# Kernel optimization log

Hardware: AMD Instinct MI355X
Metric: run time of the kernel (lower is better)

Reference implementation:

```python
import jax, jax.numpy as jnp
import numpy as np

B, T, R = 64, 256, 256          # batch, timepoints, n_rois (T==R required by bmm path)
H, NH, DH, FF, LAT, L = 256, 8, 32, 512, 64, 2
EPS = 1e-5


def layernorm(x, g, b):
    m = x.mean(-1, keepdims=True)
    v = ((x - m) ** 2).mean(-1, keepdims=True)
    return (x - m) / jnp.sqrt(v + EPS) * g + b


def leaky_relu(x):
    return jnp.where(x >= 0, x, 0.1 * x)


def setup_inputs() -> dict:
    key = jax.random.key(0)
    ks = iter(jax.random.split(key, 64))
    def nrm(shape, s=0.02):
        return jax.random.normal(next(ks), shape, jnp.float32) * s
    return {
        "x": jax.random.normal(next(ks), (B, T, R), jnp.float32),
        "node_view": jax.random.normal(next(ks), (B, R, R), jnp.float32) * 0.1,
        "edge_view": jax.random.normal(next(ks), (B, R, R), jnp.float32) * 0.1,
        "fp_w": nrm((H, R)), "fp_b": jnp.zeros((H,)),
        "fp_g": jnp.ones((H,)), "fp_beta": jnp.zeros((H,)),
        "qkv_w": nrm((L, 3 * H, H)), "qkv_b": jnp.zeros((L, 3 * H)),
        "attn_out_w": nrm((L, H, H)), "attn_out_b": jnp.zeros((L, H)),
        "ln1_g": jnp.ones((L, H)), "ln1_b": jnp.zeros((L, H)),
        "ff1_w": nrm((L, FF, H)), "ff1_b": jnp.zeros((L, FF)),
        "ff2_w": nrm((L, H, FF)), "ff2_b": jnp.zeros((L, H)),
        "ln2_g": jnp.ones((L, H)), "ln2_b": jnp.zeros((L, H)),
        "out_w": nrm((R, H)), "out_b": jnp.zeros((R,)),
        "mu_w1": nrm((H // 2, H)), "mu_b1": jnp.zeros((H // 2,)),
        "mu_g": jnp.ones((H // 2,)), "mu_beta": jnp.zeros((H // 2,)),
        "mu_w2": nrm((LAT, H // 2)), "mu_b2": jnp.zeros((LAT,)),
        "lv_w1": nrm((H // 2, H)), "lv_b1": jnp.zeros((H // 2,)),
        "lv_g": jnp.ones((H // 2,)), "lv_beta": jnp.zeros((H // 2,)),
        "lv_w2": nrm((LAT, H // 2)), "lv_b2": jnp.zeros((LAT,)),
    }


def reference(x, node_view, edge_view, fp_w, fp_b, fp_g, fp_beta,
              qkv_w, qkv_b, attn_out_w, attn_out_b, ln1_g, ln1_b,
              ff1_w, ff1_b, ff2_w, ff2_b, ln2_g, ln2_b,
              out_w, out_b, mu_w1, mu_b1, mu_g, mu_beta, mu_w2, mu_b2,
              lv_w1, lv_b1, lv_g, lv_beta, lv_w2, lv_b2):
    # graph-view message passing: bmm(x^T, view), averaged, transposed back
    xr = jnp.swapaxes(x, 1, 2)                           # [B,R,T]
    msg = 0.5 * (jnp.einsum('brt,btq->brq', xr, node_view)
                 + jnp.einsum('brt,btq->brq', xr, edge_view))
    h = jnp.swapaxes(msg, 1, 2)                          # [B,T,R]
    # feature_proj: Linear -> LayerNorm -> LeakyReLU(0.1) -> Dropout(eval)
    h = leaky_relu(layernorm(h @ fp_w.T + fp_b, fp_g, fp_beta))  # [B,T,H]
    # TransformerEncoder (post-norm, relu FFN, dropout=identity)
    scale = 1.0 / jnp.sqrt(jnp.float32(DH))
    for i in range(L):
        qkv = h @ qkv_w[i].T + qkv_b[i]                  # [B,T,3H]
        q, k, v = jnp.split(qkv, 3, axis=-1)
        q = q.reshape(B, T, NH, DH).transpose(0, 2, 1, 3)
        k = k.reshape(B, T, NH, DH).transpose(0, 2, 1, 3)
        v = v.reshape(B, T, NH, DH).transpose(0, 2, 1, 3)
        attn = jax.nn.softmax(jnp.einsum('bhqd,bhkd->bhqk', q, k) * scale, axis=-1)
        o = jnp.einsum('bhqk,bhkd->bhqd', attn, v).transpose(0, 2, 1, 3).reshape(B, T, H)
        o = o @ attn_out_w[i].T + attn_out_b[i]
        h = layernorm(h + o, ln1_g[i], ln1_b[i])
        f = jax.nn.relu(h @ ff1_w[i].T + ff1_b[i]) @ ff2_w[i].T + ff2_b[i]
        h = layernorm(h + f, ln2_g[i], ln2_b[i])
    # fresh linear (treated as fixed params) then batched Pearson correlation
    y = h @ out_w.T + out_b                              # [B,T,R]
    data = jnp.swapaxes(y, 1, 2)                         # [B,R,T]
    c = data - data.mean(-1, keepdims=True)
    std = jnp.sqrt((c ** 2).sum(-1, keepdims=True) / (T - 1))   # unbiased, like torch.std
    cn = c / (std + 1e-8)
    corr = jnp.einsum('brt,bst->brs', cn, cn) / (T - 1)
    corr = jnp.nan_to_num(jnp.clip(corr, -1.0, 1.0), nan=0.0)   # [B,R,R]
    # heads
    pooled = h.mean(axis=1)                              # [B,H]
    mu = leaky_relu(layernorm(pooled @ mu_w1.T + mu_b1, mu_g, mu_beta)) @ mu_w2.T + mu_b2
    logvar = leaky_relu(layernorm(pooled @ lv_w1.T + lv_b1, lv_g, lv_beta)) @ lv_w2.T + lv_b2
    return mu, logvar, corr
```

## Files before the change

### kernel.cpp

```cpp
#include <hip/hip_runtime.h>
#include <hip/hip_bf16.h>
#include <math.h>

#define BB 64
#define NLAYER 2

typedef __attribute__((ext_vector_type(8))) short bfrag;
typedef __attribute__((ext_vector_type(4))) float f4_t;

__device__ __forceinline__ float dot4(float4 a, float4 b, float acc) {
    acc = fmaf(a.x, b.x, acc);
    acc = fmaf(a.y, b.y, acc);
    acc = fmaf(a.z, b.z, acc);
    acc = fmaf(a.w, b.w, acc);
    return acc;
}

__device__ __forceinline__ ushort f2bf(float f) {
    uint32_t u = __float_as_uint(f);
    uint32_t r = (u + 0x7FFFu + ((u >> 16) & 1u)) >> 16;
    return (ushort)r;
}
__device__ __forceinline__ float bf2f(ushort u) {
    return __uint_as_float(((uint32_t)u) << 16);
}

__global__ __launch_bounds__(256) void k_cvt(
    const float* __restrict__ fp_w, const float* __restrict__ qkv_w,
    const float* __restrict__ aow, const float* __restrict__ f1w,
    const float* __restrict__ f2w, const float* __restrict__ outw,
    ushort* __restrict__ dst) {
    const int g = blockIdx.x;
    const size_t idx = (size_t)g * 2048 + threadIdx.x * 8;
    const float* src;
    size_t base;
    if (g < 32)       { src = fp_w;  base = 0; }
    else if (g < 224) { src = qkv_w; base = 65536; }
    else if (g < 288) { src = aow;   base = 458752; }
    else if (g < 416) { src = f1w;   base = 589824; }
    else if (g < 544) { src = f2w;   base = 851968; }
    else              { src = outw;  base = 1114112; }
    const float4* s4 = reinterpret_cast<const float4*>(src + (idx - base));
    float4 a = s4[0], b = s4[1];
    bfrag o;
    o[0] = (short)f2bf(a.x); o[1] = (short)f2bf(a.y);
    o[2] = (short)f2bf(a.z); o[3] = (short)f2bf(a.w);
    o[4] = (short)f2bf(b.x); o[5] = (short)f2bf(b.y);
    o[6] = (short)f2bf(b.z); o[7] = (short)f2bf(b.w);
    *reinterpret_cast<bfrag*>(dst + idx) = o;
}

template <int EPI, bool WF32, bool WBF>
__global__ __launch_bounds__(256) void k_mm(
    const ushort* __restrict__ A, const ushort* __restrict__ B,
    const float* __restrict__ bias, float* __restrict__ C,
    ushort* __restrict__ Cb, int K, int N,
    size_t aStr, size_t bStr, size_t cStr) {
    __shared__ __align__(16) ushort As[64 * 72];
    __shared__ __align__(16) ushort Bs[128 * 72];
    const int tid = threadIdx.x;
    const int m0 = blockIdx.x * 64, n0 = blockIdx.y * 128;
    const size_t z = blockIdx.z;
    const int w = tid >> 6, lane = tid & 63;
    const int wm = w >> 1, wn = w & 1;
    const int fr = lane & 15, fq = lane >> 4;

    const int arow = tid >> 2, akc = (tid & 3) * 16;
    const ushort* aS = A + z * aStr + (size_t)(m0 + arow) * K + akc;
    ushort* aD = &As[arow * 72 + akc];
    const int brow = tid >> 1, bkc = (tid & 1) * 32;
    const ushort* bS = B + z * bStr + (size_t)(n0 + brow) * K + bkc;
    ushort* bD = &Bs[brow * 72 + bkc];

    f4_t acc[2][4];
#pragma unroll
    for (int i = 0; i < 2; ++i)
#pragma unroll
        for (int j = 0; j < 4; ++j) acc[i][j] = (f4_t)0.f;

    bfrag ra0, ra1, rb0, rb1, rb2, rb3;
    {
        const bfrag* ap = reinterpret_cast<const bfrag*>(aS);
        ra0 = ap[0]; ra1 = ap[1];
        const bfrag* bp = reinterpret_cast<const bfrag*>(bS);
        rb0 = bp[0]; rb1 = bp[1]; rb2 = bp[2]; rb3 = bp[3];
    }

    for (int k0 = 0; k0 < K; k0 += 64) {
        reinterpret_cast<bfrag*>(aD)[0] = ra0;
        reinterpret_cast<bfrag*>(aD)[1] = ra1;
        reinterpret_cast<bfrag*>(bD)[0] = rb0;
        reinterpret_cast<bfrag*>(bD)[1] = rb1;
        reinterpret_cast<bfrag*>(bD)[2] = rb2;
        reinterpret_cast<bfrag*>(bD)[3] = rb3;
        __syncthreads();
        if (k0 + 64 < K) {
            const bfrag* ap = reinterpret_cast<const bfrag*>(aS + k0 + 64);
            ra0 = ap[0]; ra1 = ap[1];
            const bfrag* bp = reinterpret_cast<const bfrag*>(bS + k0 + 64);
            rb0 = bp[0]; rb1 = bp[1]; rb2 = bp[2]; rb3 = bp[3];
        }
#pragma unroll
        for (int ks = 0; ks < 2; ++ks) {
            const int kb = ks * 32 + fq * 8;
            bfrag af[2], bf[4];
#pragma unroll
            for (int fm = 0; fm < 2; ++fm)
                af[fm] = *reinterpret_cast<const bfrag*>(
                    &As[(wm * 32 + fm * 16 + fr) * 72 + kb]);
#pragma unroll
            for (int fn = 0; fn < 4; ++fn)
                bf[fn] = *reinterpret_cast<const bfrag*>(
                    &Bs[(wn * 64 + fn * 16 + fr) * 72 + kb]);
#pragma unroll
            for (int fm = 0; fm < 2; ++fm)
#pragma unroll
                for (int fn = 0; fn < 4; ++fn)
                    acc[fm][fn] = __builtin_amdgcn_mfma_f32_16x16x32_bf16(
                        bf[fn], af[fm], acc[fm][fn], 0, 0, 0);
        }
        __syncthreads();
    }

#pragma unroll
    for (int fn = 0; fn < 4; ++fn) {
        const int col0 = n0 + wn * 64 + fn * 16 + fq * 4;
        float4 bv = make_float4(0.f, 0.f, 0.f, 0.f);
        if (EPI != 3 && bias != nullptr)
            bv = *reinterpret_cast<const float4*>(&bias[col0]);
#pragma unroll
        for (int fm = 0; fm < 2; ++fm) {
            const int row = m0 + wm * 32 + fm * 16 + fr;
            float v0 = acc[fm][fn][0] + bv.x;
            float v1 = acc[fm][fn][1] + bv.y;
            float v2 = acc[fm][fn][2] + bv.z;
            float v3 = acc[fm][fn][3] + bv.w;
            if (EPI == 2) {
                v0 = fmaxf(v0, 0.f); v1 = fmaxf(v1, 0.f);
                v2 = fmaxf(v2, 0.f); v3 = fmaxf(v3, 0.f);
            }
            if (EPI == 3) {
                v0 = acc[fm][fn][0] * (1.f / 255.f);
                v1 = acc[fm][fn][1] * (1.f / 255.f);
                v2 = acc[fm][fn][2] * (1.f / 255.f);
                v3 = acc[fm][fn][3] * (1.f / 255.f);
                if (v0 != v0) v0 = 0.f;
                if (v1 != v1) v1 = 0.f;
                if (v2 != v2) v2 = 0.f;
                if (v3 != v3) v3 = 0.f;
                v0 = fminf(1.f, fmaxf(-1.f, v0));
                v1 = fminf(1.f, fmaxf(-1.f, v1));
                v2 = fminf(1.f, fmaxf(-1.f, v2));
                v3 = fminf(1.f, fmaxf(-1.f, v3));
            }
            const size_t o = cStr * z + (size_t)row * N + col0;
            if (WF32) {
                float4 fv = {v0, v1, v2, v3};
                *reinterpret_cast<float4*>(&C[o]) = fv;
            }
            if (WBF) {
                ushort4 uv;
                uv.x = f2bf(v0); uv.y = f2bf(v1);
                uv.z = f2bf(v2); uv.w = f2bf(v3);
                *reinterpret_cast<ushort4*>(&Cb[o]) = uv;
            }
        }
    }
}

template <int ACT, bool RES>
__global__ __launch_bounds__(256) void k_mmln(
    const ushort* __restrict__ A, const ushort* __restrict__ W,
    const float* __restrict__ bias, const ushort* __restrict__ res,
    const float* __restrict__ g, const float* __restrict__ bt,
    ushort* __restrict__ outb, int K) {
    __shared__ __align__(16) ushort As[32 * 72];
    __shared__ __align__(16) ushort Bs[256 * 72];
    __shared__ float redS[32][4];
    __shared__ float redQ[32][4];
    const int tid = threadIdx.x;
    const int m0 = blockIdx.x * 32;
    const int w = tid >> 6, lane = tid & 63;
    const int fr = lane & 15, fq = lane >> 4;

    const int arow = tid >> 3, akc = (tid & 7) * 8;
    const ushort* aS = A + (size_t)(m0 + arow) * K + akc;
    ushort* aD = &As[arow * 72 + akc];
    const int brow = tid >> 1, bkc = (tid & 1) * 32;
    const ushort* bS0 = W + (size_t)brow * K + bkc;
    const ushort* bS1 = W + (size_t)(brow + 128) * K + bkc;
    ushort* bD0 = &Bs[brow * 72 + bkc];
    ushort* bD1 = &Bs[(brow + 128) * 72 + bkc];

    f4_t acc[2][4];
#pragma unroll
    for (int i = 0; i < 2; ++i)
#pragma unroll
        for (int j = 0; j < 4; ++j) acc[i][j] = (f4_t)0.f;

    bfrag ra, rb0, rb1, rb2, rb3, rc0, rc1, rc2, rc3;
    {
        ra = *reinterpret_cast<const bfrag*>(aS);
        const bfrag* bp0 = reinterpret_cast<const bfrag*>(bS0);
        rb0 = bp0[0]; rb1 = bp0[1]; rb2 = bp0[2]; rb3 = bp0[3];
        const bfrag* bp1 = reinterpret_cast<const bfrag*>(bS1);
        rc0 = bp1[0]; rc1 = bp1[1]; rc2 = bp1[2]; rc3 = bp1[3];
    }

    for (int k0 = 0; k0 < K; k0 += 64) {
        *reinterpret_cast<bfrag*>(aD) = ra;
        reinterpret_cast<bfrag*>(bD0)[0] = rb0;
        reinterpret_cast<bfrag*>(bD0)[1] = rb1;
        reinterpret_cast<bfrag*>(bD0)[2] = rb2;
        reinterpret_cast<bfrag*>(bD0)[3] = rb3;
        reinterpret_cast<bfrag*>(bD1)[0] = rc0;
        reinterpret_cast<bfrag*>(bD1)[1] = rc1;
        reinterpret_cast<bfrag*>(bD1)[2] = rc2;
        reinterpret_cast<bfrag*>(bD1)[3] = rc3;
        __syncthreads();
        if (k0 + 64 < K) {
            ra = *reinterpret_cast<const bfrag*>(aS + k0 + 64);
            const bfrag* bp0 = reinterpret_cast<const bfrag*>(bS0 + k0 + 64);
            rb0 = bp0[0]; rb1 = bp0[1]; rb2 = bp0[2]; rb3 = bp0[3];
            const bfrag* bp1 = reinterpret_cast<const bfrag*>(bS1 + k0 + 64);
            rc0 = bp1[0]; rc1 = bp1[1]; rc2 = bp1[2]; rc3 = bp1[3];
        }
#pragma unroll
        for (int ks = 0; ks < 2; ++ks) {
            const int kb = ks * 32 + fq * 8;
            bfrag af[2], bf[4];
#pragma unroll
            for (int fm = 0; fm < 2; ++fm)
                af[fm] = *reinterpret_cast<const bfrag*>(
                    &As[(fm * 16 + fr) * 72 + kb]);
#pragma unroll
            for (int fn = 0; fn < 4; ++fn)
                bf[fn] = *reinterpret_cast<const bfrag*>(
                    &Bs[(w * 64 + fn * 16 + fr) * 72 + kb]);
#pragma unroll
            for (int fm = 0; fm < 2; ++fm)
#pragma unroll
                for (int fn = 0; fn < 4; ++fn)
                    acc[fm][fn] = __builtin_amdgcn_mfma_f32_16x16x32_bf16(
                        bf[fn], af[fm], acc[fm][fn], 0, 0, 0);
        }
        __syncthreads();
    }

#pragma unroll
    for (int fn = 0; fn < 4; ++fn) {
        const int col0 = w * 64 + fn * 16 + fq * 4;
        const float4 bv = *reinterpret_cast<const float4*>(&bias[col0]);
#pragma unroll
        for (int fm = 0; fm < 2; ++fm) {
            const int row = fm * 16 + fr;
            float r0 = 0.f, r1 = 0.f, r2 = 0.f, r3 = 0.f;
            if (RES) {
                ushort4 r4 = *reinterpret_cast<const ushort4*>(
                    &res[(size_t)(m0 + row) * 256 + col0]);
                r0 = bf2f(r4.x); r1 = bf2f(r4.y);
                r2 = bf2f(r4.z); r3 = bf2f(r4.w);
            }
            acc[fm][fn][0] += bv.x + r0;
            acc[fm][fn][1] += bv.y + r1;
            acc[fm][fn][2] += bv.z + r2;
            acc[fm][fn][3] += bv.w + r3;
        }
    }
#pragma unroll
    for (int fm = 0; fm < 2; ++fm) {
        float s = 0.f, q = 0.f;
#pragma unroll
        for (int fn = 0; fn < 4; ++fn)
#pragma unroll
            for (int j = 0; j < 4; ++j) {
                const float v = acc[fm][fn][j];
                s += v;
                q += v * v;
            }
        s += __shfl_xor(s, 16); q += __shfl_xor(q, 16);
        s += __shfl_xor(s, 32); q += __shfl_xor(q, 32);
        if (fq == 0) {
            redS[fm * 16 + fr][w] = s;
            redQ[fm * 16 + fr][w] = q;
        }
    }
    __syncthreads();
#pragma unroll
    for (int fm = 0; fm < 2; ++fm) {
        const int row = fm * 16 + fr;
        const float S = redS[row][0] + redS[row][1] + redS[row][2] + redS[row][3];
        const float Q = redQ[row][0] + redQ[row][1] + redQ[row][2] + redQ[row][3];
        const float mean = S * (1.f / 256.f);
        const float var = Q * (1.f / 256.f) - mean * mean;
        const float rstd = rsqrtf(fmaxf(var, 0.f) + 1e-5f);
        const size_t rowoff = (size_t)(m0 + row) * 256;
#pragma unroll
        for (int fn = 0; fn < 4; ++fn) {
            const int col0 = w * 64 + fn * 16 + fq * 4;
            const float4 g4 = *reinterpret_cast<const float4*>(&g[col0]);
            const float4 b4 = *reinterpret_cast<const float4*>(&bt[col0]);
            float v0 = (acc[fm][fn][0] - mean) * rstd * g4.x + b4.x;
            float v1 = (acc[fm][fn][1] - mean) * rstd * g4.y + b4.y;
            float v2 = (acc[fm][fn][2] - mean) * rstd * g4.z + b4.z;
            float v3 = (acc[fm][fn][3] - mean) * rstd * g4.w + b4.w;
            if (ACT == 1) {
                v0 = v0 >= 0.f ? v0 : 0.1f * v0;
                v1 = v1 >= 0.f ? v1 : 0.1f * v1;
                v2 = v2 >= 0.f ? v2 : 0.1f * v2;
                v3 = v3 >= 0.f ? v3 : 0.1f * v3;
            }
            ushort4 uv;
            uv.x = f2bf(v0); uv.y = f2bf(v1);
            uv.z = f2bf(v2); uv.w = f2bf(v3);
            *reinterpret_cast<ushort4*>(&outb[rowoff + col0]) = uv;
        }
    }
}

__global__ __launch_bounds__(256) void k_qkvattn(
    const ushort* __restrict__ hbuf, const ushort* __restrict__ Wqkv,
    const float* __restrict__ bias, ushort* __restrict__ o) {
    __shared__ __align__(16) ushort smem[54272];
    ushort* As = smem;
    ushort* Ws = smem + 18432;
    ushort (*Ps)[64][40] = (ushort(*)[64][40])smem;
    ushort (*Qs)[40] = (ushort(*)[40])(smem + 25344);
    ushort (*Ks)[40] = (ushort(*)[40])(smem + 35584);
    ushort (*Vt)[264] = (ushort(*)[264])(smem + 45824);

    const int hd = blockIdx.x, b = blockIdx.y;
    const int tid = threadIdx.x;
    const int w = tid >> 6, lane = tid & 63;
    const int fr = lane & 15, fq = lane >> 4;

    const ushort* aS = hbuf + (size_t)b * 65536 + (size_t)tid * 256;
    int wgrow = 0;
    if (tid < 192) {
        const int r96 = tid >> 1;
        wgrow = r96 < 32 ? hd * 32 + r96
              : (r96 < 64 ? 256 + hd * 32 + (r96 - 32)
                          : 512 + hd * 32 + (r96 - 64));
    }

    f4_t acc[4][6];
#pragma unroll
    for (int i = 0; i < 4; ++i)
#pragma unroll
        for (int j = 0; j < 6; ++j) acc[i][j] = (f4_t)0.f;

    for (int k0 = 0; k0 < 256; k0 += 64) {
        {
            const bfrag* ap = reinterpret_cast<const bfrag*>(aS + k0);
            bfrag a0 = ap[0], a1 = ap[1], a2 = ap[2], a3 = ap[3];
            bfrag a4 = ap[4], a5 = ap[5], a6 = ap[6], a7 = ap[7];
            bfrag* ad = reinterpret_cast<bfrag*>(&As[tid * 72]);
            ad[0] = a0; ad[1] = a1; ad[2] = a2; ad[3] = a3;
            ad[4] = a4; ad[5] = a5; ad[6] = a6; ad[7] = a7;
            if (tid < 192) {
                const int r96 = tid >> 1, hf = (tid & 1) * 32;
                const bfrag* wp = reinterpret_cast<const bfrag*>(
                    Wqkv + (size_t)wgrow * 256 + k0 + hf);
                bfrag w0 = wp[0], w1 = wp[1], w2 = wp[2], w3 = wp[3];
                bfrag* wd = reinterpret_cast<bfrag*>(&Ws[r96 * 72 + hf]);
                wd[0] = w0; wd[1] = w1; wd[2] = w2; wd[3] = w3;
            }
        }
        __syncthreads();
#pragma unroll
        for (int ks = 0; ks < 2; ++ks) {
            const int kb = ks * 32 + fq * 8;
            bfrag af[4], bf[6];
#pragma unroll
            for (int fm = 0; fm < 4; ++fm)
                af[fm] = *reinterpret_cast<const bfrag*>(
                    &As[(w * 64 + fm * 16 + fr) * 72 + kb]);
#pragma unroll
            for (int cf = 0; cf < 6; ++cf)
                bf[cf] = *reinterpret_cast<const bfrag*>(
                    &Ws[(cf * 16 + fr) * 72 + kb]);
#pragma unroll
            for (int fm = 0; fm < 4; ++fm)
#pragma unroll
                for (int cf = 0; cf < 6; ++cf)
                    acc[fm][cf] = __builtin_amdgcn_mfma_f32_16x16x32_bf16(
                        bf[cf], af[fm], acc[fm][cf], 0, 0, 0);
        }
        __syncthreads();
    }

#pragma unroll
    for (int cf = 0; cf < 6; ++cf) {
        const int c0 = cf * 16 + fq * 4;
        const int cl = c0 & 31;
        const int gbase = (cf < 2) ? hd * 32 + cl
                        : (cf < 4) ? 256 + hd * 32 + cl
                                   : 512 + hd * 32 + cl;
        const float4 bv = *reinterpret_cast<const float4*>(&bias[gbase]);
#pragma unroll
        for (int fm = 0; fm < 4; ++fm) {
            const int row = w * 64 + fm * 16 + fr;
            float v0 = acc[fm][cf][0] + bv.x;
            float v1 = acc[fm][cf][1] + bv.y;
            float v2 = acc[fm][cf][2] + bv.z;
            float v3 = acc[fm][cf][3] + bv.w;
            if (cf < 2) {
                ushort4 uv;
                uv.x = f2bf(v0); uv.y = f2bf(v1);
                uv.z = f2bf(v2); uv.w = f2bf(v3);
                *reinterpret_cast<ushort4*>(&Qs[row][cl]) = uv;
            } else if (cf < 4) {
                ushort4 uv;
                uv.x = f2bf(v0); uv.y = f2bf(v1);
                uv.z = f2bf(v2); uv.w = f2bf(v3);
                *reinterpret_cast<ushort4*>(&Ks[row][cl]) = uv;
            } else {
                Vt[cl + 0][row] = f2bf(v0);
                Vt[cl + 1][row] = f2bf(v1);
                Vt[cl + 2][row] = f2bf(v2);
                Vt[cl + 3][row] = f2bf(v3);
            }
        }
    }
    __syncthreads();

    const int q0 = w * 64;
    bfrag qf[4];
#pragma unroll
    for (int fm = 0; fm < 4; ++fm)
        qf[fm] = *reinterpret_cast<const bfrag*>(&Qs[q0 + fm * 16 + fr][fq * 8]);

    f4_t oacc[4][2];
    float rs[4][4];
#pragma unroll
    for (int fm = 0; fm < 4; ++fm) {
        oacc[fm][0] = (f4_t)0.f;
        oacc[fm][1] = (f4_t)0.f;
#pragma unroll
        for (int j = 0; j < 4; ++j) rs[fm][j] = 0.f;
    }
    const f4_t zero4 = (f4_t)0.f;
    const float qsl = 0.17677669529663687f * 1.4426950408889634f;

    for (int kt = 0; kt < 8; ++kt) {
        bfrag kf0 = *reinterpret_cast<const bfrag*>(&Ks[kt * 32 + fr][fq * 8]);
        bfrag kf1 = *reinterpret_cast<const bfrag*>(&Ks[kt * 32 + 16 + fr][fq * 8]);
        f4_t s0[4], s1[4];
#pragma unroll
        for (int fm = 0; fm < 4; ++fm) {
            s0[fm] = __builtin_amdgcn_mfma_f32_16x16x32_bf16(qf[fm], kf0, zero4, 0, 0, 0);
            s1[fm] = __builtin_amdgcn_mfma_f32_16x16x32_bf16(qf[fm], kf1, zero4, 0, 0, 0);
        }
#pragma unroll
        for (int fm = 0; fm < 4; ++fm) {
#pragma unroll
            for (int j = 0; j < 4; ++j) {
                const int row = fm * 16 + fq * 4 + j;
                ushort u0 = f2bf(exp2f(s0[fm][j] * qsl));
                ushort u1 = f2bf(exp2f(s1[fm][j] * qsl));
                Ps[w][row][fr] = u0;
                Ps[w][row][16 + fr] = u1;
                rs[fm][j] += bf2f(u0) + bf2f(u1);
            }
        }
        bfrag vf0 = *reinterpret_cast<const bfrag*>(&Vt[fr][kt * 32 + fq * 8]);
        bfrag vf1 = *reinterpret_cast<const bfrag*>(&Vt[16 + fr][kt * 32 + fq * 8]);
        bfrag pf[4];
#pragma unroll
        for (int fm = 0; fm < 4; ++fm)
            pf[fm] = *reinterpret_cast<const bfrag*>(&Ps[w][fm * 16 + fr][fq * 8]);
#pragma unroll
        for (int fm = 0; fm < 4; ++fm) {
            oacc[fm][0] = __builtin_amdgcn_mfma_f32_16x16x32_bf16(pf[fm], vf0, oacc[fm][0], 0, 0, 0);
            oacc[fm][1] = __builtin_amdgcn_mfma_f32_16x16x32_bf16(pf[fm], vf1, oacc[fm][1], 0, 0, 0);
        }
    }

#pragma unroll
    for (int fm = 0; fm < 4; ++fm)
#pragma unroll
        for (int j = 0; j < 4; ++j) {
            float r = rs[fm][j];
            r += __shfl_xor(r, 1);
            r += __shfl_xor(r, 2);
            r += __shfl_xor(r, 4);
            r += __shfl_xor(r, 8);
            rs[fm][j] = 1.f / r;
        }
    ushort* ob = o + (size_t)b * 65536 + hd * 32;
#pragma unroll
    for (int fm = 0; fm < 4; ++fm) {
        const int qrow = q0 + fm * 16 + fq * 4;
#pragma unroll
        for (int j = 0; j < 4; ++j) {
            const float inv = rs[fm][j];
            ob[(size_t)(qrow + j) * 256 + fr] = f2bf(oacc[fm][0][j] * inv);
            ob[(size_t)(qrow + j) * 256 + 16 + fr] = f2bf(oacc[fm][1][j] * inv);
        }
    }
}

__global__ __launch_bounds__(256) void k_xpose_bmm(
    const float* __restrict__ x, const float* __restrict__ nv,
    const float* __restrict__ ev, ushort* __restrict__ At,
    ushort* __restrict__ Xt) {
    const int b = blockIdx.z;
    const int k0 = blockIdx.x * 64, i0 = blockIdx.y * 64;
    __shared__ float TA[64][65];
    __shared__ float TX[64][65];
    const size_t bb = (size_t)b * 65536;
    const int tid = threadIdx.x;
    const int lr = tid >> 4, lc = (tid & 15) * 4;
#pragma unroll
    for (int l = 0; l < 4; ++l) {
        const int row = lr + l * 16;
        const size_t gidx = bb + (size_t)(k0 + row) * 256 + i0 + lc;
        float4 n4 = *reinterpret_cast<const float4*>(nv + gidx);
        float4 e4 = *reinterpret_cast<const float4*>(ev + gidx);
        float4 x4 = *reinterpret_cast<const float4*>(x + gidx);
        TA[row][lc] = 0.5f * (n4.x + e4.x);
        TA[row][lc + 1] = 0.5f * (n4.y + e4.y);
        TA[row][lc + 2] = 0.5f * (n4.z + e4.z);
        TA[row][lc + 3] = 0.5f * (n4.w + e4.w);
        TX[row][lc] = x4.x;
        TX[row][lc + 1] = x4.y;
        TX[row][lc + 2] = x4.z;
        TX[row][lc + 3] = x4.w;
    }
    __syncthreads();
    const int i = tid & 63, kk = (tid >> 6) * 16;
    bfrag a0, a1, x0, x1;
#pragma unroll
    for (int e = 0; e < 8; ++e) {
        a0[e] = (short)f2bf(TA[kk + e][i]);
        a1[e] = (short)f2bf(TA[kk + 8 + e][i]);
        x0[e] = (short)f2bf(TX[kk + e][i]);
        x1[e] = (short)f2bf(TX[kk + 8 + e][i]);
    }
    const size_t o = bb + (size_t)(i0 + i) * 256 + k0 + kk;
    *reinterpret_cast<bfrag*>(At + o) = a0;
    *reinterpret_cast<bfrag*>(At + o + 8) = a1;
    *reinterpret_cast<bfrag*>(Xt + o) = x0;
    *reinterpret_cast<bfrag*>(Xt + o + 8) = x1;
}

__global__ __launch_bounds__(256) void k_pstats(const ushort* __restrict__ y,
                                                ushort* __restrict__ cnT) {
    const int b = blockIdx.y, r0 = blockIdx.x * 64;
    __shared__ __align__(16) ushort T[256][72];
    __shared__ float sred[4][64];
    __shared__ float qred[4][64];
    __shared__ float mstat[64];
    __shared__ float istat[64];
    const int tid = threadIdx.x;
    {
        const bfrag* yv = reinterpret_cast<const bfrag*>(
            y + (size_t)b * 65536 + (size_t)tid * 256 + r0);
#pragma unroll
        for (int i = 0; i < 8; ++i)
            *reinterpret_cast<bfrag*>(&T[tid][i * 8]) = yv[i];
    }
    __syncthreads();
    const int rl = tid & 63, tc = tid >> 6;
    {
        float s = 0.f, q = 0.f;
        for (int t = 0; t < 64; ++t) {
            float v = bf2f(T[tc * 64 + t][rl]);
            s += v;
            q += v * v;
        }
        sred[tc][rl] = s;
        qred[tc][rl] = q;
    }
    __syncthreads();
    if (tid < 64) {
        const float S = sred[0][tid] + sred[1][tid] + sred[2][tid] + sred[3][tid];
        const float Q = qred[0][tid] + qred[1][tid] + qred[2][tid] + qred[3][tid];
        const float mean = S * (1.f / 256.f);
        const float var = (Q - S * mean) * (1.f / 255.f);
        const float stdv = sqrtf(fmaxf(var, 0.f));
        mstat[tid] = mean;
        istat[tid] = 1.f / (stdv + 1e-8f);
    }
    __syncthreads();
    const float mean = mstat[rl], inv = istat[rl];
    ushort* dst = cnT + (size_t)b * 65536 + (size_t)(r0 + rl) * 256 + tc * 64;
#pragma unroll
    for (int i = 0; i < 8; ++i) {
        bfrag c;
#pragma unroll
        for (int e = 0; e < 8; ++e)
            c[e] = (short)f2bf((bf2f(T[tc * 64 + i * 8 + e][rl]) - mean) * inv);
        reinterpret_cast<bfrag*>(dst)[i] = c;
    }
}

__global__ __launch_bounds__(512) void k_poolhead(
    const ushort* __restrict__ h,
    const float* __restrict__ mw1, const float* __restrict__ mb1,
    const float* __restrict__ mg, const float* __restrict__ mbt,
    const float* __restrict__ mw2, const float* __restrict__ mb2,
    const float* __restrict__ lw1, const float* __restrict__ lb1,
    const float* __restrict__ lg, const float* __restrict__ lbt,
    const float* __restrict__ lw2, const float* __restrict__ lb2,
    float* __restrict__ outp) {
    const int b = blockIdx.x, tid = threadIdx.x;
    __shared__ float pp[2][256];
    __shared__ float pooled[256];
    __shared__ float rS[4], rQ[4];
    __shared__ float t1[2][128];

    {
        const int c = tid & 255, tc = tid >> 8;
        const ushort* hb = h + (size_t)b * 65536 + (size_t)tc * 128 * 256 + c;
        float s = 0.f;
        for (int t = 0; t < 128; ++t) s += bf2f(hb[(size_t)t * 256]);
        pp[tc][c] = s;
    }
    __syncthreads();
    if (tid < 256) pooled[tid] = (pp[0][tid] + pp[1][tid]) * (1.f / 256.f);
    __syncthreads();

    float a = 0.f;
    if (tid < 256) {
        const int hd = tid >> 7, u = tid & 127;
        const float* w1 = hd ? lw1 : mw1;
        const float* b1 = hd ? lb1 : mb1;
        a = b1[u];
        const float4* w1v = reinterpret_cast<const float4*>(w1 + (size_t)u * 256);
#pragma unroll 4
        for (int k4 = 0; k4 < 64; ++k4) {
            float4 wv = w1v[k4];
            float4 p = *reinterpret_cast<const float4*>(&pooled[k4 * 4]);
            a = dot4(p, wv, a);
        }
        float s = a, q = a * a;
#pragma unroll
        for (int m = 1; m < 64; m <<= 1) {
            s += __shfl_xor(s, m);
            q += __shfl_xor(q, m);
        }
        if ((tid & 63) == 0) { rS[tid >> 6] = s; rQ[tid >> 6] = q; }
    }
    __syncthreads();
    if (tid < 256) {
        const int hd = tid >> 7, u = tid & 127;
        const float* g = hd ? lg : mg;
        const float* bt = hd ? lbt : mbt;
        const float S = rS[hd * 2] + rS[hd * 2 + 1];
        const float Q = rQ[hd * 2] + rQ[hd * 2 + 1];
        const float mean = S * (1.f / 128.f);
        const float var = Q * (1.f / 128.f) - mean * mean;
        const float rstd = rsqrtf(fmaxf(var, 0.f) + 1e-5f);
        float v = (a - mean) * rstd * g[u] + bt[u];
        v = v >= 0.f ? v : 0.1f * v;
        t1[hd][u] = v;
    }
    __syncthreads();
    if (tid < 128) {
        const int hd = tid >> 6, ou = tid & 63;
        const float* w2 = hd ? lw2 : mw2;
        const float* b2 = hd ? lb2 : mb2;
        float o = b2[ou];
        const float* w2r = w2 + (size_t)ou * 128;
#pragma unroll 4
        for (int c = 0; c < 128; ++c) o = fmaf(t1[hd][c], w2r[c], o);
        outp[hd * 4096 + b * 64 + ou] = o;
    }
}

extern "C" void kernel_launch(void* const* d_in, const int* in_sizes, int n_in,
                              void* d_out, int out_size, void* d_ws, size_t ws_size,
                              hipStream_t stream) {
    const float* x = (const float*)d_in[0];
    const float* nv = (const float*)d_in[1];
    const float* ev = (const float*)d_in[2];
    const float* fp_w = (const float*)d_in[3];
    const float* fp_b = (const float*)d_in[4];
    const float* fp_g = (const float*)d_in[5];
    const float* fp_beta = (const float*)d_in[6];
    const float* qkv_w = (const float*)d_in[7];
    const float* qkv_b = (const float*)d_in[8];
    const float* aow = (const float*)d_in[9];
    const float* aob = (const float*)d_in[10];
    const float* ln1g = (const float*)d_in[11];
    const float* ln1b = (const float*)d_in[12];
    const float* f1w = (const float*)d_in[13];
    const float* f1b = (const float*)d_in[14];
    const float* f2w = (const float*)d_in[15];
    const float* f2b = (const float*)d_in[16];
    const float* ln2g = (const float*)d_in[17];
    const float* ln2b = (const float*)d_in[18];
    const float* outw = (const float*)d_in[19];
    const float* outb = (const float*)d_in[20];
    const float* muw1 = (const float*)d_in[21];
    const float* mub1 = (const float*)d_in[22];
    const float* mug = (const float*)d_in[23];
    const float* mubt = (const float*)d_in[24];
    const float* muw2 = (const float*)d_in[25];
    const float* mub2 = (const float*)d_in[26];
    const float* lvw1 = (const float*)d_in[27];
    const float* lvb1 = (const float*)d_in[28];
    const float* lvg = (const float*)d_in[29];
    const float* lvbt = (const float*)d_in[30];
    const float* lvw2 = (const float*)d_in[31];
    const float* lvb2 = (const float*)d_in[32];

    float* out = (float*)d_out;
    float* ws = (float*)d_ws;

    ushort* ub = (ushort*)ws;
    ushort* wh_bf = ub;
    ushort* At = ub + 4194304;
    ushort* Xt = ub + 8388608;
    ushort* o_bf = ub + 16777216;
    ushort* h0_bf = o_bf;
    ushort* f1_bf = ub + 20971520;
    ushort* cnT = f1_bf;
    ushort* y_bf = ub + 29360128;
    ushort* wbf = ub + 33554432;

    k_cvt<<<576, 256, 0, stream>>>(fp_w, qkv_w, aow, f1w, f2w, outw, wbf);

    k_xpose_bmm<<<dim3(4, 4, BB), 256, 0, stream>>>(x, nv, ev, At, Xt);
    k_mm<0, false, true><<<dim3(4, 2, BB), 256, 0, stream>>>(
        At, Xt, nullptr, nullptr, h0_bf, 256, 256, 65536, 65536, 65536);

    k_mmln<1, false><<<512, 256, 0, stream>>>(
        h0_bf, wbf, fp_b, nullptr, fp_g, fp_beta, wh_bf, 256);

    for (int l = 0; l < NLAYER; ++l) {
        k_qkvattn<<<dim3(8, BB), 256, 0, stream>>>(
            wh_bf, wbf + 65536 + (size_t)l * 196608, qkv_b + l * 768, o_bf);
        k_mmln<0, true><<<512, 256, 0, stream>>>(
            o_bf, wbf + 458752 + (size_t)l * 65536, aob + l * 256,
            wh_bf, ln1g + l * 256, ln1b + l * 256, wh_bf, 256);
        k_mm<2, false, true><<<dim3(256, 4, 1), 256, 0, stream>>>(
            wh_bf, wbf + 589824 + (size_t)l * 131072, f1b + l * 512,
            nullptr, f1_bf, 256, 512, 0, 0, 0);
        k_mmln<0, true><<<512, 256, 0, stream>>>(
            f1_bf, wbf + 851968 + (size_t)l * 131072, f2b + l * 256,
            wh_bf, ln2g + l * 256, ln2b + l * 256, wh_bf, 512);
    }

    k_mm<0, false, true><<<dim3(256, 2, 1), 256, 0, stream>>>(
        wh_bf, wbf + 1114112, outb, nullptr, y_bf, 256, 256, 0, 0, 0);

    k_pstats<<<dim3(4, BB), 256, 0, stream>>>(y_bf, cnT);
    k_mm<3, true, false><<<dim3(4, 2, BB), 256, 0, stream>>>(
        cnT, cnT, nullptr, out + 8192, nullptr, 256, 256, 65536, 65536, 65536);

    k_poolhead<<<BB, 512, 0, stream>>>(
        wh_bf, muw1, mub1, mug, mubt, muw2, mub2,
        lvw1, lvb1, lvg, lvbt, lvw2, lvb2, out);
}
```

Measured before the change: 261.3 us.

## Split QKV projection from attention and fold Pearson centering into correlation epilogue

The fused per-head QKV+attention kernel is replaced by a standalone tiled GEMM that writes Q, K and transposed V to global memory. A separate attention kernel then reads its fragments straight from global/L2 instead of LDS. The output projection now produces y already transposed, and a light row-stats kernel computes mean and inverse std. The correlation GEMM runs on raw y and applies mean and std correction in its epilogue, removing the normalized-copy pass and the out bias (which centering cancels). The trade-offs are more global traffic for Q/K/V, an extra launch per layer, and possible cancellation error from the uncentered bf16 Gram product.

```diff
diff --git a/kernel.cpp b/kernel.cpp
--- a/kernel.cpp
+++ b/kernel.cpp
@@ -126,7 +126,7 @@
     for (int fn = 0; fn < 4; ++fn) {
         const int col0 = n0 + wn * 64 + fn * 16 + fq * 4;
         float4 bv = make_float4(0.f, 0.f, 0.f, 0.f);
-        if (EPI != 3 && bias != nullptr)
+        if (bias != nullptr)
             bv = *reinterpret_cast<const float4*>(&bias[col0]);
 #pragma unroll
         for (int fm = 0; fm < 2; ++fm) {
@@ -138,20 +138,6 @@
             if (EPI == 2) {
                 v0 = fmaxf(v0, 0.f); v1 = fmaxf(v1, 0.f);
                 v2 = fmaxf(v2, 0.f); v3 = fmaxf(v3, 0.f);
-            }
-            if (EPI == 3) {
-                v0 = acc[fm][fn][0] * (1.f / 255.f);
-                v1 = acc[fm][fn][1] * (1.f / 255.f);
-                v2 = acc[fm][fn][2] * (1.f / 255.f);
-                v3 = acc[fm][fn][3] * (1.f / 255.f);
-                if (v0 != v0) v0 = 0.f;
-                if (v1 != v1) v1 = 0.f;
-                if (v2 != v2) v2 = 0.f;
-                if (v3 != v3) v3 = 0.f;
-                v0 = fminf(1.f, fmaxf(-1.f, v0));
-                v1 = fminf(1.f, fmaxf(-1.f, v1));
-                v2 = fminf(1.f, fmaxf(-1.f, v2));
-                v3 = fminf(1.f, fmaxf(-1.f, v3));
             }
             const size_t o = cStr * z + (size_t)row * N + col0;
             if (WF32) {
@@ -163,6 +149,108 @@
                 uv.x = f2bf(v0); uv.y = f2bf(v1);
                 uv.z = f2bf(v2); uv.w = f2bf(v3);
                 *reinterpret_cast<ushort4*>(&Cb[o]) = uv;
+            }
+        }
+    }
+}
+
+__global__ __launch_bounds__(256) void k_mmqkv(
+    const ushort* __restrict__ A, const ushort* __restrict__ B,
+    const float* __restrict__ bias, ushort* __restrict__ qb,
+    ushort* __restrict__ kbuf, ushort* __restrict__ vtb) {
+    __shared__ __align__(16) ushort As[64 * 72];
+    __shared__ __align__(16) ushort Bs[128 * 72];
+    const int tid = threadIdx.x;
+    const int m0 = blockIdx.x * 64, n0 = blockIdx.y * 128;
+    const int w = tid >> 6, lane = tid & 63;
+    const int wm = w >> 1, wn = w & 1;
+    const int fr = lane & 15, fq = lane >> 4;
+    const int K = 256;
+
+    const int arow = tid >> 2, akc = (tid & 3) * 16;
+    const ushort* aS = A + (size_t)(m0 + arow) * K + akc;
+    ushort* aD = &As[arow * 72 + akc];
+    const int brow = tid >> 1, bkc = (tid & 1) * 32;
+    const ushort* bS = B + (size_t)(n0 + brow) * K + bkc;
+    ushort* bD = &Bs[brow * 72 + bkc];
+
+    f4_t acc[2][4];
+#pragma unroll
+    for (int i = 0; i < 2; ++i)
+#pragma unroll
+        for (int j = 0; j < 4; ++j) acc[i][j] = (f4_t)0.f;
+
+    bfrag ra0, ra1, rb0, rb1, rb2, rb3;
+    {
+        const bfrag* ap = reinterpret_cast<const bfrag*>(aS);
+        ra0 = ap[0]; ra1 = ap[1];
+        const bfrag* bp = reinterpret_cast<const bfrag*>(bS);
+        rb0 = bp[0]; rb1 = bp[1]; rb2 = bp[2]; rb3 = bp[3];
+    }
+
+    for (int k0 = 0; k0 < K; k0 += 64) {
+        reinterpret_cast<bfrag*>(aD)[0] = ra0;
+        reinterpret_cast<bfrag*>(aD)[1] = ra1;
+        reinterpret_cast<bfrag*>(bD)[0] = rb0;
+        reinterpret_cast<bfrag*>(bD)[1] = rb1;
+        reinterpret_cast<bfrag*>(bD)[2] = rb2;
+        reinterpret_cast<bfrag*>(bD)[3] = rb3;
+        __syncthreads();
+        if (k0 + 64 < K) {
+            const bfrag* ap = reinterpret_cast<const bfrag*>(aS + k0 + 64);
+            ra0 = ap[0]; ra1 = ap[1];
+            const bfrag* bp = reinterpret_cast<const bfrag*>(bS + k0 + 64);
+            rb0 = bp[0]; rb1 = bp[1]; rb2 = bp[2]; rb3 = bp[3];
+        }
+#pragma unroll
+        for (int ks = 0; ks < 2; ++ks) {
+            const int kb = ks * 32 + fq * 8;
+            bfrag af[2], bf[4];
+#pragma unroll
+            for (int fm = 0; fm < 2; ++fm)
+                af[fm] = *reinterpret_cast<const bfrag*>(
+                    &As[(wm * 32 + fm * 16 + fr) * 72 + kb]);
+#pragma unroll
+            for (int fn = 0; fn < 4; ++fn)
+                bf[fn] = *reinterpret_cast<const bfrag*>(
+                    &Bs[(wn * 64 + fn * 16 + fr) * 72 + kb]);
+#pragma unroll
+            for (int fm = 0; fm < 2; ++fm)
+#pragma unroll
+                for (int fn = 0; fn < 4; ++fn)
+                    acc[fm][fn] = __builtin_amdgcn_mfma_f32_16x16x32_bf16(
+                        bf[fn], af[fm], acc[fm][fn], 0, 0, 0);
+        }
+        __syncthreads();
+    }
+
+    const int sec = n0 >> 8;
+#pragma unroll
+    for (int fn = 0; fn < 4; ++fn) {
+        const int col0 = n0 + wn * 64 + fn * 16 + fq * 4;
+        const int hd = (col0 >> 5) & 7, dq = col0 & 31;
+        const float4 bv = *reinterpret_cast<const float4*>(&bias[col0]);
+#pragma unroll
+        for (int fm = 0; fm < 2; ++fm) {
+            const int row = m0 + wm * 32 + fm * 16 + fr;
+            const int b = row >> 8, t = row & 255;
+            const size_t bh = (size_t)b * 8 + hd;
+            float v0 = acc[fm][fn][0] + bv.x;
+            float v1 = acc[fm][fn][1] + bv.y;
+            float v2 = acc[fm][fn][2] + bv.z;
+            float v3 = acc[fm][fn][3] + bv.w;
+            if (sec < 2) {
+                ushort4 uv;
+                uv.x = f2bf(v0); uv.y = f2bf(v1);
+                uv.z = f2bf(v2); uv.w = f2bf(v3);
+                ushort* dst = (sec == 0 ? qb : kbuf) + (bh * 256 + t) * 32 + dq;
+                *reinterpret_cast<ushort4*>(dst) = uv;
+            } else {
+                ushort* dst = vtb + (bh * 32 + dq) * 256 + t;
+                dst[0] = f2bf(v0);
+                dst[256] = f2bf(v1);
+                dst[512] = f2bf(v2);
+                dst[768] = f2bf(v3);
             }
         }
     }
@@ -318,117 +406,26 @@
     }
 }
 
-__global__ __launch_bounds__(256) void k_qkvattn(
-    const ushort* __restrict__ hbuf, const ushort* __restrict__ Wqkv,
-    const float* __restrict__ bias, ushort* __restrict__ o) {
-    __shared__ __align__(16) ushort smem[54272];
-    ushort* As = smem;
-    ushort* Ws = smem + 18432;
-    ushort (*Ps)[64][40] = (ushort(*)[64][40])smem;
-    ushort (*Qs)[40] = (ushort(*)[40])(smem + 25344);
-    ushort (*Ks)[40] = (ushort(*)[40])(smem + 35584);
-    ushort (*Vt)[264] = (ushort(*)[264])(smem + 45824);
-
+__global__ __launch_bounds__(256) void k_attn3(
+    const ushort* __restrict__ qb, const ushort* __restrict__ kbuf,
+    const ushort* __restrict__ vtb, ushort* __restrict__ o) {
+    __shared__ __align__(16) ushort Ps[4][64][40];
     const int hd = blockIdx.x, b = blockIdx.y;
+    const size_t bh = (size_t)b * 8 + hd;
     const int tid = threadIdx.x;
     const int w = tid >> 6, lane = tid & 63;
     const int fr = lane & 15, fq = lane >> 4;
 
-    const ushort* aS = hbuf + (size_t)b * 65536 + (size_t)tid * 256;
-    int wgrow = 0;
-    if (tid < 192) {
-        const int r96 = tid >> 1;
-        wgrow = r96 < 32 ? hd * 32 + r96
-              : (r96 < 64 ? 256 + hd * 32 + (r96 - 32)
-                          : 512 + hd * 32 + (r96 - 64));
-    }
-
-    f4_t acc[4][6];
-#pragma unroll
-    for (int i = 0; i < 4; ++i)
-#pragma unroll
-        for (int j = 0; j < 6; ++j) acc[i][j] = (f4_t)0.f;
-
-    for (int k0 = 0; k0 < 256; k0 += 64) {
-        {
-            const bfrag* ap = reinterpret_cast<const bfrag*>(aS + k0);
-            bfrag a0 = ap[0], a1 = ap[1], a2 = ap[2], a3 = ap[3];
-            bfrag a4 = ap[4], a5 = ap[5], a6 = ap[6], a7 = ap[7];
-            bfrag* ad = reinterpret_cast<bfrag*>(&As[tid * 72]);
-            ad[0] = a0; ad[1] = a1; ad[2] = a2; ad[3] = a3;
-            ad[4] = a4; ad[5] = a5; ad[6] = a6; ad[7] = a7;
-            if (tid < 192) {
-                const int r96 = tid >> 1, hf = (tid & 1) * 32;
-                const bfrag* wp = reinterpret_cast<const bfrag*>(
-                    Wqkv + (size_t)wgrow * 256 + k0 + hf);
-                bfrag w0 = wp[0], w1 = wp[1], w2 = wp[2], w3 = wp[3];
-                bfrag* wd = reinterpret_cast<bfrag*>(&Ws[r96 * 72 + hf]);
-                wd[0] = w0; wd[1] = w1; wd[2] = w2; wd[3] = w3;
-            }
-        }
-        __syncthreads();
-#pragma unroll
-        for (int ks = 0; ks < 2; ++ks) {
-            const int kb = ks * 32 + fq * 8;
-            bfrag af[4], bf[6];
-#pragma unroll
-            for (int fm = 0; fm < 4; ++fm)
-                af[fm] = *reinterpret_cast<const bfrag*>(
-                    &As[(w * 64 + fm * 16 + fr) * 72 + kb]);
-#pragma unroll
-            for (int cf = 0; cf < 6; ++cf)
-                bf[cf] = *reinterpret_cast<const bfrag*>(
-                    &Ws[(cf * 16 + fr) * 72 + kb]);
-#pragma unroll
-            for (int fm = 0; fm < 4; ++fm)
-#pragma unroll
-                for (int cf = 0; cf < 6; ++cf)
-                    acc[fm][cf] = __builtin_amdgcn_mfma_f32_16x16x32_bf16(
-                        bf[cf], af[fm], acc[fm][cf], 0, 0, 0);
-        }
-        __syncthreads();
-    }
-
-#pragma unroll
-    for (int cf = 0; cf < 6; ++cf) {
-        const int c0 = cf * 16 + fq * 4;
-        const int cl = c0 & 31;
-        const int gbase = (cf < 2) ? hd * 32 + cl
-                        : (cf < 4) ? 256 + hd * 32 + cl
-                                   : 512 + hd * 32 + cl;
-        const float4 bv = *reinterpret_cast<const float4*>(&bias[gbase]);
-#pragma unroll
-        for (int fm = 0; fm < 4; ++fm) {
-            const int row = w * 64 + fm * 16 + fr;
-            float v0 = acc[fm][cf][0] + bv.x;
-            float v1 = acc[fm][cf][1] + bv.y;
-            float v2 = acc[fm][cf][2] + bv.z;
-            float v3 = acc[fm][cf][3] + bv.w;
-            if (cf < 2) {
-                ushort4 uv;
-                uv.x = f2bf(v0); uv.y = f2bf(v1);
-                uv.z = f2bf(v2); uv.w = f2bf(v3);
-                *reinterpret_cast<ushort4*>(&Qs[row][cl]) = uv;
-            } else if (cf < 4) {
-                ushort4 uv;
-                uv.x = f2bf(v0); uv.y = f2bf(v1);
-                uv.z = f2bf(v2); uv.w = f2bf(v3);
-                *reinterpret_cast<ushort4*>(&Ks[row][cl]) = uv;
-            } else {
-                Vt[cl + 0][row] = f2bf(v0);
-                Vt[cl + 1][row] = f2bf(v1);
-                Vt[cl + 2][row] = f2bf(v2);
-                Vt[cl + 3][row] = f2bf(v3);
-            }
-        }
-    }
-    __syncthreads();
+    const ushort* qB = qb + bh * 8192;
+    const ushort* kB = kbuf + bh * 8192;
+    const ushort* vB = vtb + bh * 8192;
 
     const int q0 = w * 64;
     bfrag qf[4];
 #pragma unroll
     for (int fm = 0; fm < 4; ++fm)
-        qf[fm] = *reinterpret_cast<const bfrag*>(&Qs[q0 + fm * 16 + fr][fq * 8]);
+        qf[fm] = *reinterpret_cast<const bfrag*>(
+            qB + (size_t)(q0 + fm * 16 + fr) * 32 + fq * 8);
 
     f4_t oacc[4][2];
     float rs[4][4];
@@ -443,8 +440,10 @@
     const float qsl = 0.17677669529663687f * 1.4426950408889634f;
 
     for (int kt = 0; kt < 8; ++kt) {
-        bfrag kf0 = *reinterpret_cast<const bfrag*>(&Ks[kt * 32 + fr][fq * 8]);
-        bfrag kf1 = *reinterpret_cast<const bfrag*>(&Ks[kt * 32 + 16 + fr][fq * 8]);
+        bfrag kf0 = *reinterpret_cast<const bfrag*>(
+            kB + (size_t)(kt * 32 + fr) * 32 + fq * 8);
+        bfrag kf1 = *reinterpret_cast<const bfrag*>(
+            kB + (size_t)(kt * 32 + 16 + fr) * 32 + fq * 8);
         f4_t s0[4], s1[4];
 #pragma unroll
         for (int fm = 0; fm < 4; ++fm) {
@@ -463,8 +462,10 @@
                 rs[fm][j] += bf2f(u0) + bf2f(u1);
             }
         }
-        bfrag vf0 = *reinterpret_cast<const bfrag*>(&Vt[fr][kt * 32 + fq * 8]);
-        bfrag vf1 = *reinterpret_cast<const bfrag*>(&Vt[16 + fr][kt * 32 + fq * 8]);
+        bfrag vf0 = *reinterpret_cast<const bfrag*>(
+            vB + (size_t)fr * 256 + kt * 32 + fq * 8);
+        bfrag vf1 = *reinterpret_cast<const bfrag*>(
+            vB + (size_t)(16 + fr) * 256 + kt * 32 + fq * 8);
         bfrag pf[4];
 #pragma unroll
         for (int fm = 0; fm < 4; ++fm)
@@ -544,54 +545,131 @@
     *reinterpret_cast<bfrag*>(Xt + o + 8) = x1;
 }
 
-__global__ __launch_bounds__(256) void k_pstats(const ushort* __restrict__ y,
-                                                ushort* __restrict__ cnT) {
-    const int b = blockIdx.y, r0 = blockIdx.x * 64;
-    __shared__ __align__(16) ushort T[256][72];
-    __shared__ float sred[4][64];
-    __shared__ float qred[4][64];
-    __shared__ float mstat[64];
-    __shared__ float istat[64];
+__global__ __launch_bounds__(256) void k_rowstats(const ushort* __restrict__ yT,
+                                                  float* __restrict__ stats) {
+    const int b = blockIdx.y;
+    const int r = blockIdx.x * 64 + (threadIdx.x >> 2);
+    const int part = threadIdx.x & 3;
+    const ushort* row = yT + (size_t)b * 65536 + (size_t)r * 256 + part * 64;
+    float s = 0.f, q = 0.f;
+#pragma unroll
+    for (int i = 0; i < 8; ++i) {
+        bfrag v = reinterpret_cast<const bfrag*>(row)[i];
+#pragma unroll
+        for (int e = 0; e < 8; ++e) {
+            float f = bf2f((ushort)v[e]);
+            s += f;
+            q += f * f;
+        }
+    }
+    s += __shfl_xor(s, 1); q += __shfl_xor(q, 1);
+    s += __shfl_xor(s, 2); q += __shfl_xor(q, 2);
+    if (part == 0) {
+        const float mean = s * (1.f / 256.f);
+        const float var = (q - s * mean) * (1.f / 255.f);
+        const float stdv = sqrtf(fmaxf(var, 0.f));
+        stats[b * 512 + r] = mean;
+        stats[b * 512 + 256 + r] = 1.f / (stdv + 1e-8f);
+    }
+}
+
+__global__ __launch_bounds__(256) void k_corr2(
+    const ushort* __restrict__ A, const float* __restrict__ stats,
+    float* __restrict__ C) {
+    __shared__ __align__(16) ushort As[64 * 72];
+    __shared__ __align__(16) ushort Bs[128 * 72];
     const int tid = threadIdx.x;
+    const int m0 = blockIdx.x * 64, n0 = blockIdx.y * 128;
+    const size_t z = blockIdx.z;
+    const int w = tid >> 6, lane = tid & 63;
+    const int wm = w >> 1, wn = w & 1;
+    const int fr = lane & 15, fq = lane >> 4;
+    const int K = 256;
+
+    const int arow = tid >> 2, akc = (tid & 3) * 16;
+    const ushort* aS = A + z * 65536 + (size_t)(m0 + arow) * K + akc;
+    ushort* aD = &As[arow * 72 + akc];
+    const int brow = tid >> 1, bkc = (tid & 1) * 32;
+    const ushort* bS = A + z * 65536 + (size_t)(n0 + brow) * K + bkc;
+    ushort* bD = &Bs[brow * 72 + bkc];
+
+    f4_t acc[2][4];
+#pragma unroll
+    for (int i = 0; i < 2; ++i)
+#pragma unroll
+        for (int j = 0; j < 4; ++j) acc[i][j] = (f4_t)0.f;
+
+    bfrag ra0, ra1, rb0, rb1, rb2, rb3;
     {
-        const bfrag* yv = reinterpret_cast<const bfrag*>(
-            y + (size_t)b * 65536 + (size_t)tid * 256 + r0);
-#pragma unroll
-        for (int i = 0; i < 8; ++i)
-            *reinterpret_cast<bfrag*>(&T[tid][i * 8]) = yv[i];
-    }
-    __syncthreads();
-    const int rl = tid & 63, tc = tid >> 6;
-    {
-        float s = 0.f, q = 0.f;
-        for (int t = 0; t < 64; ++t) {
-            float v = bf2f(T[tc * 64 + t][rl]);
-            s += v;
-            q += v * v;
-        }
-        sred[tc][rl] = s;
-        qred[tc][rl] = q;
-    }
-    __syncthreads();
-    if (tid < 64) {
-        const float S = sred[0][tid] + sred[1][tid] + sred[2][tid] + sred[3][tid];
-        const float Q = qred[0][tid] + qred[1][tid] + qred[2][tid] + qred[3][tid];
-        const float mean = S * (1.f / 256.f);
-        const float var = (Q - S * mean) * (1.f / 255.f);
-        const float stdv = sqrtf(fmaxf(var, 0.f));
-        mstat[tid] = mean;
-        istat[tid] = 1.f / (stdv + 1e-8f);
-    }
-    __syncthreads();
-    const float mean = mstat[rl], inv = istat[rl];
-    ushort* dst = cnT + (size_t)b * 65536 + (size_t)(r0 + rl) * 256 + tc * 64;
-#pragma unroll
-    for (int i = 0; i < 8; ++i) {
-        bfrag c;
-#pragma unroll
-        for (int e = 0; e < 8; ++e)
-            c[e] = (short)f2bf((bf2f(T[tc * 64 + i * 8 + e][rl]) - mean) * inv);
-        reinterpret_cast<bfrag*>(dst)[i] = c;
+        const bfrag* ap = reinterpret_cast<const bfrag*>(aS);
+        ra0 = ap[0]; ra1 = ap[1];
+        const bfrag* bp = reinterpret_cast<const bfrag*>(bS);
+        rb0 = bp[0]; rb1 = bp[1]; rb2 = bp[2]; rb3 = bp[3];
+    }
+
+    for (int k0 = 0; k0 < K; k0 += 64) {
+        reinterpret_cast<bfrag*>(aD)[0] = ra0;
+        reinterpret_cast<bfrag*>(aD)[1] = ra1;
+        reinterpret_cast<bfrag*>(bD)[0] = rb0;
+        reinterpret_cast<bfrag*>(bD)[1] = rb1;
+        reinterpret_cast<bfrag*>(bD)[2] = rb2;
+        reinterpret_cast<bfrag*>(bD)[3] = rb3;
+        __syncthreads();
+        if (k0 + 64 < K) {
+            const bfrag* ap = reinterpret_cast<const bfrag*>(aS + k0 + 64);
+            ra0 = ap[0]; ra1 = ap[1];
+            const bfrag* bp = reinterpret_cast<const bfrag*>(bS + k0 + 64);
+            rb0 = bp[0]; rb1 = bp[1]; rb2 = bp[2]; rb3 = bp[3];
+        }
+#pragma unroll
+        for (int ks = 0; ks < 2; ++ks) {
+            const int kb = ks * 32 + fq * 8;
+            bfrag af[2], bf[4];
+#pragma unroll
+            for (int fm = 0; fm < 2; ++fm)
+                af[fm] = *reinterpret_cast<const bfrag*>(
+                    &As[(wm * 32 + fm * 16 + fr) * 72 + kb]);
+#pragma unroll
+            for (int fn = 0; fn < 4; ++fn)
+                bf[fn] = *reinterpret_cast<const bfrag*>(
+                    &Bs[(wn * 64 + fn * 16 + fr) * 72 + kb]);
+#pragma unroll
+            for (int fm = 0; fm < 2; ++fm)
+#pragma unroll
+                for (int fn = 0; fn < 4; ++fn)
+                    acc[fm][fn] = __builtin_amdgcn_mfma_f32_16x16x32_bf16(
+                        bf[fn], af[fm], acc[fm][fn], 0, 0, 0);
+        }
+        __syncthreads();
+    }
+
+    const float* st = stats + z * 512;
+#pragma unroll
+    for (int fn = 0; fn < 4; ++fn) {
+        const int col0 = n0 + wn * 64 + fn * 16 + fq * 4;
+        const float4 muj = *reinterpret_cast<const float4*>(&st[col0]);
+        const float4 isj = *reinterpret_cast<const float4*>(&st[256 + col0]);
+#pragma unroll
+        for (int fm = 0; fm < 2; ++fm) {
+            const int row = m0 + wm * 32 + fm * 16 + fr;
+            const float mui = st[row];
+            const float isi = st[256 + row] * (1.f / 255.f);
+            float v0 = (acc[fm][fn][0] - 256.f * mui * muj.x) * isi * isj.x;
+            float v1 = (acc[fm][fn][1] - 256.f * mui * muj.y) * isi * isj.y;
+            float v2 = (acc[fm][fn][2] - 256.f * mui * muj.z) * isi * isj.z;
+            float v3 = (acc[fm][fn][3] - 256.f * mui * muj.w) * isi * isj.w;
+            if (v0 != v0) v0 = 0.f;
+            if (v1 != v1) v1 = 0.f;
+            if (v2 != v2) v2 = 0.f;
+            if (v3 != v3) v3 = 0.f;
+            v0 = fminf(1.f, fmaxf(-1.f, v0));
+            v1 = fminf(1.f, fmaxf(-1.f, v1));
+            v2 = fminf(1.f, fmaxf(-1.f, v2));
+            v3 = fminf(1.f, fmaxf(-1.f, v3));
+            float4 fv = {v0, v1, v2, v3};
+            *reinterpret_cast<float4*>(
+                &C[z * 65536 + (size_t)row * 256 + col0]) = fv;
+        }
     }
 }
 
@@ -709,16 +787,19 @@
     float* out = (float*)d_out;
     float* ws = (float*)d_ws;
 
-    ushort* ub = (ushort*)ws;
+    float* stats = ws;
+    ushort* ub = (ushort*)(ws + 32768);
     ushort* wh_bf = ub;
     ushort* At = ub + 4194304;
     ushort* Xt = ub + 8388608;
     ushort* o_bf = ub + 16777216;
     ushort* h0_bf = o_bf;
     ushort* f1_bf = ub + 20971520;
-    ushort* cnT = f1_bf;
-    ushort* y_bf = ub + 29360128;
-    ushort* wbf = ub + 33554432;
+    ushort* qb = ub + 29360128;
+    ushort* kb = ub + 33554432;
+    ushort* vtb = ub + 37748736;
+    ushort* yT = ub + 41943040;
+    ushort* wbf = ub + 46137344;
 
     k_cvt<<<576, 256, 0, stream>>>(fp_w, qkv_w, aow, f1w, f2w, outw, wbf);
 
@@ -730,8 +811,10 @@
         h0_bf, wbf, fp_b, nullptr, fp_g, fp_beta, wh_bf, 256);
 
     for (int l = 0; l < NLAYER; ++l) {
-        k_qkvattn<<<dim3(8, BB), 256, 0, stream>>>(
-            wh_bf, wbf + 65536 + (size_t)l * 196608, qkv_b + l * 768, o_bf);
+        k_mmqkv<<<dim3(256, 6), 256, 0, stream>>>(
+            wh_bf, wbf + 65536 + (size_t)l * 196608, qkv_b + l * 768,
+            qb, kb, vtb);
+        k_attn3<<<dim3(8, BB), 256, 0, stream>>>(qb, kb, vtb, o_bf);
         k_mmln<0, true><<<512, 256, 0, stream>>>(
             o_bf, wbf + 458752 + (size_t)l * 65536, aob + l * 256,
             wh_bf, ln1g + l * 256, ln1b + l * 256, wh_bf, 256);
@@ -743,12 +826,11 @@
             wh_bf, ln2g + l * 256, ln2b + l * 256, wh_bf, 512);
     }
 
-    k_mm<0, false, true><<<dim3(256, 2, 1), 256, 0, stream>>>(
-        wh_bf, wbf + 1114112, outb, nullptr, y_bf, 256, 256, 0, 0, 0);
-
-    k_pstats<<<dim3(4, BB), 256, 0, stream>>>(y_bf, cnT);
-    k_mm<3, true, false><<<dim3(4, 2, BB), 256, 0, stream>>>(
-        cnT, cnT, nullptr, out + 8192, nullptr, 256, 256, 65536, 65536, 65536);
+    k_mm<0, false, true><<<dim3(4, 2, BB), 256, 0, stream>>>(
+        wbf + 1114112, wh_bf, nullptr, nullptr, yT, 256, 256, 0, 65536, 65536);
+
+    k_rowstats<<<dim3(4, BB), 256, 0, stream>>>(yT, stats);
+    k_corr2<<<dim3(4, 2, BB), 256, 0, stream>>>(yT, stats, out + 8192);
 
     k_poolhead<<<BB, 512, 0, stream>>>(
         wh_bf, muw1, mub1, mug, mubt, muw2, mub2,
```

Result: faster. 239.1 us (-8.5%).
